# Optimization experiments

Hardware: AMD Instinct MI355X
Metric: run time of the kernel (lower is better)

Reference implementation:

```python
import jax, jax.numpy as jnp
import numpy as np

EPS = 1e-5

def _layernorm(x, g, b):
    m = jnp.mean(x, axis=-1, keepdims=True)
    v = jnp.mean((x - m) ** 2, axis=-1, keepdims=True)
    return (x - m) * jax.lax.rsqrt(v + EPS) * g + b

def setup_inputs() -> dict:
    N, D, R = 1024, 128, 64
    dist_mean = 60.0
    key = jax.random.key(0)
    ks = jax.random.split(key, 12)
    def lin(k, fan_in, shape):
        bound = 1.0 / np.sqrt(fan_in)
        return jax.random.uniform(k, shape, jnp.float32, -bound, bound)
    inp = {
        "node_emb": jax.random.normal(ks[0], (N, D), jnp.float32),
        # src_proj: Linear(D, R) + LayerNorm(R)
        "w_src": lin(ks[1], D, (R, D)), "b_src": lin(ks[2], D, (R,)),
        "g_src": jnp.ones((R,), jnp.float32), "be_src": jnp.zeros((R,), jnp.float32),
        # dst_proj: Linear(D, R) + LayerNorm(R)
        "w_dst": lin(ks[3], D, (R, D)), "b_dst": lin(ks[4], D, (R,)),
        "g_dst": jnp.ones((R,), jnp.float32), "be_dst": jnp.zeros((R,), jnp.float32),
        # scorer: Linear(3R, 2R) -> ReLU -> Linear(2R, R) -> ReLU -> Linear(R, 1)
        "w1": lin(ks[5], 3 * R, (2 * R, 3 * R)), "b1": lin(ks[6], 3 * R, (2 * R,)),
        "w2": lin(ks[7], 2 * R, (R, 2 * R)), "b2": lin(ks[8], 2 * R, (R,)),
        "w3": lin(ks[9], R, (1, R)) * 0.01, "b3": jnp.full((1,), dist_mean, jnp.float32),
    }
    return inp

def reference(node_emb, w_src, b_src, g_src, be_src, w_dst, b_dst, g_dst, be_dst,
              w1, b1, w2, b2, w3, b3):
    # src/dst projections: [N, R]
    src = jax.nn.relu(_layernorm(node_emb @ w_src.T + b_src, g_src, be_src))
    dst = jax.nn.relu(_layernorm(node_emb @ w_dst.T + b_dst, g_dst, be_dst))
    N = node_emb.shape[0]
    # broadcast pairwise features: [N, N, 3R]
    src_exp = jnp.broadcast_to(src[:, None, :], (N, N, src.shape[-1]))
    dst_exp = jnp.broadcast_to(dst[None, :, :], (N, N, dst.shape[-1]))
    pair = jnp.concatenate([src_exp, dst_exp, src_exp * dst_exp], axis=-1)
    h = jax.nn.relu(pair @ w1.T + b1)   # [N, N, 2R]
    h = jax.nn.relu(h @ w2.T + b2)      # [N, N, R]
    cost = (h @ w3.T + b3)[..., 0]      # [N, N]
    return cost
```

## Files before the change

kernel.cpp:

```cpp
#include <hip/hip_runtime.h>

typedef _Float16 half2v __attribute__((ext_vector_type(2)));
typedef _Float16 half8v __attribute__((ext_vector_type(8)));
typedef float f32x4 __attribute__((ext_vector_type(4)));
typedef unsigned uint2v __attribute__((ext_vector_type(2)));

__device__ inline half2v cvt_pk(float a, float b) {
    return __builtin_bit_cast(half2v, __builtin_amdgcn_cvt_pkrtz(a, b));
}
__device__ inline half2v pkmax0(half2v x) {
    half2v r;
    asm("v_pk_max_f16 %0, %1, 0" : "=v"(r) : "v"(x));
    return r;
}
__device__ inline unsigned short f16bits(float f) {
    _Float16 h = (_Float16)f;
    return __builtin_bit_cast(unsigned short, h);
}
__device__ inline unsigned packf16(float a, float b) {
    return (unsigned)f16bits(a) | ((unsigned)f16bits(b) << 16);
}
__device__ inline float lo16(unsigned u) {
    return (float)__builtin_bit_cast(_Float16, (unsigned short)(u & 0xffffu));
}
__device__ inline float hi16(unsigned u) {
    return (float)__builtin_bit_cast(_Float16, (unsigned short)(u >> 16));
}

__global__ __launch_bounds__(256) void proj_kernel(
    const float* __restrict__ node,
    const float* __restrict__ w_src, const float* __restrict__ b_src,
    const float* __restrict__ g_src, const float* __restrict__ be_src,
    const float* __restrict__ w_dst, const float* __restrict__ b_dst,
    const float* __restrict__ g_dst, const float* __restrict__ be_dst,
    const float* __restrict__ w1, const float* __restrict__ b1,
    const float* __restrict__ w2, const float* __restrict__ w3,
    unsigned short* __restrict__ src_f16, unsigned short* __restrict__ dst_f16,
    float* __restrict__ A1, unsigned short* __restrict__ B1h,
    unsigned short* __restrict__ w1c_frag, unsigned short* __restrict__ w2_frag,
    unsigned short* __restrict__ w3p)
{
    __shared__ unsigned sWh[64 * 65];
    __shared__ unsigned sw1h[128 * 33];
    __shared__ float snode[4][128];
    __shared__ float sy[4][64];

    const int tid = threadIdx.x;
    const int wloc = tid >> 6;
    const int lane = tid & 63;
    const int gw = blockIdx.x * 4 + wloc;
    const int row = gw & 1023;
    const int kind = gw >> 10;

    const float* W  = kind ? w_dst  : w_src;
    const float* Bv = kind ? b_dst  : b_src;
    const float* G  = kind ? g_dst  : g_src;
    const float* BE = kind ? be_dst : be_src;
    const int koff = kind * 64;

    #pragma unroll
    for (int u = 0; u < 16; u++) {
        int w = u * 256 + tid;
        int r = w >> 6, c2 = w & 63;
        float2 v = *(const float2*)(W + r * 128 + c2 * 2);
        sWh[r * 65 + c2] = packf16(v.x, v.y);
    }
    #pragma unroll
    for (int u = 0; u < 16; u++) {
        int w = u * 256 + tid;
        int r = w >> 5, c2 = w & 31;
        float2 v = *(const float2*)(w1 + (size_t)r * 192 + koff + c2 * 2);
        sw1h[r * 33 + c2] = packf16(v.x, v.y);
    }
    snode[wloc][lane]      = node[row * 128 + lane];
    snode[wloc][lane + 64] = node[row * 128 + 64 + lane];
    __syncthreads();

    float acc = Bv[lane];
    #pragma unroll 8
    for (int k2 = 0; k2 < 64; k2++) {
        unsigned wp = sWh[lane * 65 + k2];
        float2 nv = *(const float2*)&snode[wloc][2 * k2];
        acc += nv.x * lo16(wp) + nv.y * hi16(wp);
    }

    float s = acc;
    #pragma unroll
    for (int off = 32; off >= 1; off >>= 1) s += __shfl_xor(s, off);
    float mean = s * (1.0f / 64.0f);
    float d = acc - mean;
    float ss = d * d;
    #pragma unroll
    for (int off = 32; off >= 1; off >>= 1) ss += __shfl_xor(ss, off);
    float rstd = rsqrtf(ss * (1.0f / 64.0f) + 1e-5f);
    float y = fmaxf(d * rstd * G[lane] + BE[lane], 0.0f);

    unsigned short* obf = kind ? dst_f16 : src_f16;
    obf[row * 64 + lane] = f16bits(y);

    sy[wloc][lane] = y;
    __builtin_amdgcn_s_waitcnt(0);

    float a0 = kind ? 0.0f : b1[lane];
    float a1 = kind ? 0.0f : b1[lane + 64];
    #pragma unroll 8
    for (int k2 = 0; k2 < 32; k2++) {
        float2 yv = *(const float2*)&sy[wloc][2 * k2];
        unsigned wa = sw1h[lane * 33 + k2];
        unsigned wb = sw1h[(lane + 64) * 33 + k2];
        a0 += yv.x * lo16(wa) + yv.y * hi16(wa);
        a1 += yv.x * lo16(wb) + yv.y * hi16(wb);
    }
    if (kind == 0) {
        A1[row * 128 + lane] = a0;
        A1[row * 128 + lane + 64] = a1;
    } else {
        B1h[row * 128 + lane] = f16bits(a0);
        B1h[row * 128 + lane + 64] = f16bits(a1);
    }

    if (blockIdx.x < 8) {
        int t = blockIdx.x * 256 + threadIdx.x;
        int which = t >> 10;
        int idx = t & 1023;
        int f = idx >> 6, l = idx & 63;
        int lqq = l >> 4, lrr = l & 15;
        if (which == 0) {
            int mt = f >> 1, kt = f & 1;
            #pragma unroll
            for (int e = 0; e < 8; e++)
                w1c_frag[idx * 8 + e] =
                    f16bits(w1[(size_t)(mt * 16 + lrr) * 192 + 128 + kt * 32 + lqq * 8 + e]);
        } else {
            int mt2 = f >> 2, kt2 = f & 3;
            #pragma unroll
            for (int e = 0; e < 8; e++) {
                int col = (2 * kt2 + (e >> 2)) * 16 + lqq * 4 + (e & 3);
                w2_frag[idx * 8 + e] =
                    f16bits(w2[(size_t)(mt2 * 16 + lrr) * 128 + col]);
            }
        }
    } else if (blockIdx.x == 8 && threadIdx.x < 64) {
        int l = threadIdx.x;
        int kt = l >> 5, rem = l & 31, lqq = rem >> 3, ee = rem & 7;
        w3p[l] = f16bits(w3[(2 * kt + (ee >> 2)) * 16 + lqq * 4 + (ee & 3)]);
    }
}

__global__ __launch_bounds__(256, 2) void pair_kernel(
    const unsigned short* __restrict__ src_f16, const unsigned short* __restrict__ dst_f16,
    const float* __restrict__ A1, const unsigned short* __restrict__ B1h,
    const unsigned short* __restrict__ w1c_frag, const unsigned short* __restrict__ w2_frag,
    const unsigned short* __restrict__ w3p, const float* __restrict__ b2,
    const float* __restrict__ b3, float* __restrict__ out)
{
    __shared__ __align__(16) float sA1[32][128];
    __shared__ __align__(16) unsigned short sSrc[32][64];

    const int tid = threadIdx.x;
    const int wv = tid >> 6;
    const int lane = tid & 63;
    const int lq = lane >> 4, lr = lane & 15;
    const int i0 = blockIdx.y * 32, j0 = blockIdx.x * 32;
    const int ibase = (wv & 1) * 16;
    const int jbase = j0 + (wv >> 1) * 16;

    #pragma unroll
    for (int u = 0; u < 4; u++) {
        int idx = u * 256 + tid;
        int r = idx >> 5, c = (idx & 31) * 4;
        *(f32x4*)&sA1[r][c] = *(const f32x4*)(A1 + (size_t)(i0 + r) * 128 + c);
    }
    {
        int r = tid >> 3, c = (tid & 7) * 8;
        *(uint4*)&sSrc[r][c] = *(const uint4*)(src_f16 + (size_t)(i0 + r) * 64 + c);
    }

    half8v w1f[8][2], w2f[4][4], w3f[2];
    {
        const uint4* gw1 = (const uint4*)w1c_frag;
        #pragma unroll
        for (int mt = 0; mt < 8; mt++)
            #pragma unroll
            for (int kt = 0; kt < 2; kt++)
                w1f[mt][kt] = __builtin_bit_cast(half8v, gw1[(mt * 2 + kt) * 64 + lane]);
        const uint4* gw2 = (const uint4*)w2_frag;
        #pragma unroll
        for (int mt2 = 0; mt2 < 4; mt2++)
            #pragma unroll
            for (int kt = 0; kt < 4; kt++)
                w2f[mt2][kt] = __builtin_bit_cast(half8v, gw2[(mt2 * 4 + kt) * 64 + lane]);
        #pragma unroll
        for (int kt = 0; kt < 2; kt++)
            w3f[kt] = *(const half8v*)(w3p + kt * 32 + lq * 8);
    }
    f32x4 b2v[4];
    #pragma unroll
    for (int mt2 = 0; mt2 < 4; mt2++)
        b2v[mt2] = *(const f32x4*)(b2 + mt2 * 16 + lq * 4);
    const float b3s = b3[0];
    const f32x4 b3c = {b3s, b3s, b3s, b3s};

    const int j = jbase + lr;
    half8v dstf0, dstf1;
    {
        const uint4* drow = (const uint4*)(dst_f16 + (size_t)j * 64);
        dstf0 = __builtin_bit_cast(half8v, drow[lq]);
        dstf1 = __builtin_bit_cast(half8v, drow[4 + lq]);
    }
    half2v b1pk[8][2];
    #pragma unroll
    for (int mt = 0; mt < 8; mt++) {
        uint2v bl = *(const uint2v*)(B1h + (size_t)j * 128 + mt * 16 + lq * 4);
        b1pk[mt][0] = __builtin_bit_cast(half2v, bl[0]);
        b1pk[mt][1] = __builtin_bit_cast(half2v, bl[1]);
    }

    __syncthreads();

    for (int cc = 0; cc < 16; cc++) {
        const int i_loc = ibase + cc;
        const int i = i0 + i_loc;
        const half8v s0 = *(const half8v*)&sSrc[i_loc][lq * 8];
        const half8v s1 = *(const half8v*)&sSrc[i_loc][32 + lq * 8];
        f32x4 acc1[8];
        #pragma unroll
        for (int mt = 0; mt < 8; mt++)
            acc1[mt] = *(const f32x4*)&sA1[i_loc][mt * 16 + lq * 4];
        const half8v c0 = s0 * dstf0;
        const half8v c1 = s1 * dstf1;
        #pragma unroll
        for (int mt = 0; mt < 8; mt++) {
            acc1[mt] = __builtin_amdgcn_mfma_f32_16x16x32_f16(w1f[mt][0], c0, acc1[mt], 0, 0, 0);
            acc1[mt] = __builtin_amdgcn_mfma_f32_16x16x32_f16(w1f[mt][1], c1, acc1[mt], 0, 0, 0);
        }
        unsigned P[16];
        #pragma unroll
        for (int mt = 0; mt < 8; mt++) {
            half2v p0 = cvt_pk(acc1[mt][0], acc1[mt][1]) + b1pk[mt][0];
            half2v p1 = cvt_pk(acc1[mt][2], acc1[mt][3]) + b1pk[mt][1];
            P[mt * 2 + 0] = __builtin_bit_cast(unsigned, pkmax0(p0));
            P[mt * 2 + 1] = __builtin_bit_cast(unsigned, pkmax0(p1));
        }
        f32x4 acc2[4];
        {
            uint4 hb = {P[0], P[1], P[2], P[3]};
            half8v hf = __builtin_bit_cast(half8v, hb);
            #pragma unroll
            for (int mt2 = 0; mt2 < 4; mt2++)
                acc2[mt2] = __builtin_amdgcn_mfma_f32_16x16x32_f16(w2f[mt2][0], hf, b2v[mt2], 0, 0, 0);
        }
        #pragma unroll
        for (int kt = 1; kt < 4; kt++) {
            uint4 hb = {P[4 * kt], P[4 * kt + 1], P[4 * kt + 2], P[4 * kt + 3]};
            half8v hf = __builtin_bit_cast(half8v, hb);
            #pragma unroll
            for (int mt2 = 0; mt2 < 4; mt2++)
                acc2[mt2] = __builtin_amdgcn_mfma_f32_16x16x32_f16(w2f[mt2][kt], hf, acc2[mt2], 0, 0, 0);
        }
        unsigned P2[8];
        #pragma unroll
        for (int mt2 = 0; mt2 < 4; mt2++) {
            P2[mt2 * 2 + 0] = __builtin_bit_cast(unsigned, pkmax0(cvt_pk(acc2[mt2][0], acc2[mt2][1])));
            P2[mt2 * 2 + 1] = __builtin_bit_cast(unsigned, pkmax0(cvt_pk(acc2[mt2][2], acc2[mt2][3])));
        }
        uint4 h20 = {P2[0], P2[1], P2[2], P2[3]};
        uint4 h21 = {P2[4], P2[5], P2[6], P2[7]};
        f32x4 acc3 = __builtin_amdgcn_mfma_f32_16x16x32_f16(
            w3f[0], __builtin_bit_cast(half8v, h20), b3c, 0, 0, 0);
        acc3 = __builtin_amdgcn_mfma_f32_16x16x32_f16(
            w3f[1], __builtin_bit_cast(half8v, h21), acc3, 0, 0, 0);
        if (lane < 16)
            out[(size_t)i * 1024 + jbase + lane] = acc3[0];
    }
}

extern "C" void kernel_launch(void* const* d_in, const int* in_sizes, int n_in,
                              void* d_out, int out_size, void* d_ws, size_t ws_size,
                              hipStream_t stream) {
    (void)in_sizes; (void)n_in; (void)out_size; (void)ws_size;
    const float* node   = (const float*)d_in[0];
    const float* w_src  = (const float*)d_in[1];
    const float* b_src  = (const float*)d_in[2];
    const float* g_src  = (const float*)d_in[3];
    const float* be_src = (const float*)d_in[4];
    const float* w_dst  = (const float*)d_in[5];
    const float* b_dst  = (const float*)d_in[6];
    const float* g_dst  = (const float*)d_in[7];
    const float* be_dst = (const float*)d_in[8];
    const float* w1     = (const float*)d_in[9];
    const float* b1     = (const float*)d_in[10];
    const float* w2     = (const float*)d_in[11];
    const float* b2     = (const float*)d_in[12];
    const float* w3     = (const float*)d_in[13];
    const float* b3     = (const float*)d_in[14];

    char* ws = (char*)d_ws;
    unsigned short* src_f16  = (unsigned short*)(ws);
    unsigned short* dst_f16  = (unsigned short*)(ws + 131072);
    float*          A1       = (float*)(ws + 262144);
    unsigned short* B1h      = (unsigned short*)(ws + 786432);
    unsigned short* w1c_frag = (unsigned short*)(ws + 1310720);
    unsigned short* w2_frag  = (unsigned short*)(ws + 1327104);
    unsigned short* w3p      = (unsigned short*)(ws + 1343488);

    hipLaunchKernelGGL(proj_kernel, dim3(512), dim3(256), 0, stream,
                       node, w_src, b_src, g_src, be_src, w_dst, b_dst, g_dst, be_dst,
                       w1, b1, w2, w3, src_f16, dst_f16, A1, B1h,
                       w1c_frag, w2_frag, w3p);
    hipLaunchKernelGGL(pair_kernel, dim3(32, 32), dim3(256), 0, stream,
                       src_f16, dst_f16, A1, B1h, w1c_frag, w2_frag, w3p, b2, b3,
                       (float*)d_out);
}
```

Baseline: 42.41 us.

## Move B1/b2/w3 operands to LDS and replace final MFMA with shuffle reduction

Per-lane register copies of the B1 bias fragments and b2 are dropped; the pair kernel now stages B1 rows, b2 and w3 in shared memory and reads them inside the loop. The last linear layer (h @ w3) no longer uses an f16 MFMA. It becomes an fp32 dot product of the ReLU'd accumulators with w3, followed by two cross-lane shuffles. The aim is lower VGPR pressure and fewer MFMA and convert instructions, at the cost of extra LDS reads every iteration. The w3 repack step in the projection kernel is removed.

```diff
diff --git a/kernel.cpp b/kernel.cpp
--- a/kernel.cpp
+++ b/kernel.cpp
@@ -34,11 +34,10 @@
     const float* __restrict__ w_dst, const float* __restrict__ b_dst,
     const float* __restrict__ g_dst, const float* __restrict__ be_dst,
     const float* __restrict__ w1, const float* __restrict__ b1,
-    const float* __restrict__ w2, const float* __restrict__ w3,
+    const float* __restrict__ w2,
     unsigned short* __restrict__ src_f16, unsigned short* __restrict__ dst_f16,
     float* __restrict__ A1, unsigned short* __restrict__ B1h,
-    unsigned short* __restrict__ w1c_frag, unsigned short* __restrict__ w2_frag,
-    unsigned short* __restrict__ w3p)
+    unsigned short* __restrict__ w1c_frag, unsigned short* __restrict__ w2_frag)
 {
     __shared__ unsigned sWh[64 * 65];
     __shared__ unsigned sw1h[128 * 33];
@@ -140,10 +139,6 @@
                     f16bits(w2[(size_t)(mt2 * 16 + lrr) * 128 + col]);
             }
         }
-    } else if (blockIdx.x == 8 && threadIdx.x < 64) {
-        int l = threadIdx.x;
-        int kt = l >> 5, rem = l & 31, lqq = rem >> 3, ee = rem & 7;
-        w3p[l] = f16bits(w3[(2 * kt + (ee >> 2)) * 16 + lqq * 4 + (ee & 3)]);
     }
 }
 
@@ -151,11 +146,14 @@
     const unsigned short* __restrict__ src_f16, const unsigned short* __restrict__ dst_f16,
     const float* __restrict__ A1, const unsigned short* __restrict__ B1h,
     const unsigned short* __restrict__ w1c_frag, const unsigned short* __restrict__ w2_frag,
-    const unsigned short* __restrict__ w3p, const float* __restrict__ b2,
+    const float* __restrict__ b2, const float* __restrict__ w3,
     const float* __restrict__ b3, float* __restrict__ out)
 {
     __shared__ __align__(16) float sA1[32][128];
     __shared__ __align__(16) unsigned short sSrc[32][64];
+    __shared__ __align__(16) unsigned short sB1[32][136];
+    __shared__ __align__(16) float sB2[128];
+    __shared__ __align__(16) float sW3[64];
 
     const int tid = threadIdx.x;
     const int wv = tid >> 6;
@@ -163,7 +161,8 @@
     const int lq = lane >> 4, lr = lane & 15;
     const int i0 = blockIdx.y * 32, j0 = blockIdx.x * 32;
     const int ibase = (wv & 1) * 16;
-    const int jbase = j0 + (wv >> 1) * 16;
+    const int jl_base = (wv >> 1) * 16;
+    const int jbase = j0 + jl_base;
 
     #pragma unroll
     for (int u = 0; u < 4; u++) {
@@ -175,8 +174,16 @@
         int r = tid >> 3, c = (tid & 7) * 8;
         *(uint4*)&sSrc[r][c] = *(const uint4*)(src_f16 + (size_t)(i0 + r) * 64 + c);
     }
-
-    half8v w1f[8][2], w2f[4][4], w3f[2];
+    #pragma unroll
+    for (int u = 0; u < 2; u++) {
+        int idx = u * 256 + tid;
+        int r = idx >> 4, c = (idx & 15) * 8;
+        *(uint4*)&sB1[r][c] = *(const uint4*)(B1h + (size_t)(j0 + r) * 128 + c);
+    }
+    if (tid < 32) *(f32x4*)&sB2[tid * 4] = *(const f32x4*)(b2 + tid * 4);
+    else if (tid < 48) *(f32x4*)&sW3[(tid - 32) * 4] = *(const f32x4*)(w3 + (tid - 32) * 4);
+
+    half8v w1f[8][2], w2f[4][4];
     {
         const uint4* gw1 = (const uint4*)w1c_frag;
         #pragma unroll
@@ -190,16 +197,8 @@
             #pragma unroll
             for (int kt = 0; kt < 4; kt++)
                 w2f[mt2][kt] = __builtin_bit_cast(half8v, gw2[(mt2 * 4 + kt) * 64 + lane]);
-        #pragma unroll
-        for (int kt = 0; kt < 2; kt++)
-            w3f[kt] = *(const half8v*)(w3p + kt * 32 + lq * 8);
-    }
-    f32x4 b2v[4];
-    #pragma unroll
-    for (int mt2 = 0; mt2 < 4; mt2++)
-        b2v[mt2] = *(const f32x4*)(b2 + mt2 * 16 + lq * 4);
+    }
     const float b3s = b3[0];
-    const f32x4 b3c = {b3s, b3s, b3s, b3s};
 
     const int j = jbase + lr;
     half8v dstf0, dstf1;
@@ -208,13 +207,7 @@
         dstf0 = __builtin_bit_cast(half8v, drow[lq]);
         dstf1 = __builtin_bit_cast(half8v, drow[4 + lq]);
     }
-    half2v b1pk[8][2];
-    #pragma unroll
-    for (int mt = 0; mt < 8; mt++) {
-        uint2v bl = *(const uint2v*)(B1h + (size_t)j * 128 + mt * 16 + lq * 4);
-        b1pk[mt][0] = __builtin_bit_cast(half2v, bl[0]);
-        b1pk[mt][1] = __builtin_bit_cast(half2v, bl[1]);
-    }
+    const int jl = jl_base + lr;
 
     __syncthreads();
 
@@ -237,8 +230,9 @@
         unsigned P[16];
         #pragma unroll
         for (int mt = 0; mt < 8; mt++) {
-            half2v p0 = cvt_pk(acc1[mt][0], acc1[mt][1]) + b1pk[mt][0];
-            half2v p1 = cvt_pk(acc1[mt][2], acc1[mt][3]) + b1pk[mt][1];
+            uint2v bl = *(const uint2v*)&sB1[jl][mt * 16 + lq * 4];
+            half2v p0 = cvt_pk(acc1[mt][0], acc1[mt][1]) + __builtin_bit_cast(half2v, bl[0]);
+            half2v p1 = cvt_pk(acc1[mt][2], acc1[mt][3]) + __builtin_bit_cast(half2v, bl[1]);
             P[mt * 2 + 0] = __builtin_bit_cast(unsigned, pkmax0(p0));
             P[mt * 2 + 1] = __builtin_bit_cast(unsigned, pkmax0(p1));
         }
@@ -247,8 +241,10 @@
             uint4 hb = {P[0], P[1], P[2], P[3]};
             half8v hf = __builtin_bit_cast(half8v, hb);
             #pragma unroll
-            for (int mt2 = 0; mt2 < 4; mt2++)
-                acc2[mt2] = __builtin_amdgcn_mfma_f32_16x16x32_f16(w2f[mt2][0], hf, b2v[mt2], 0, 0, 0);
+            for (int mt2 = 0; mt2 < 4; mt2++) {
+                f32x4 b2t = *(const f32x4*)&sB2[mt2 * 16 + lq * 4];
+                acc2[mt2] = __builtin_amdgcn_mfma_f32_16x16x32_f16(w2f[mt2][0], hf, b2t, 0, 0, 0);
+            }
         }
         #pragma unroll
         for (int kt = 1; kt < 4; kt++) {
@@ -258,20 +254,18 @@
             for (int mt2 = 0; mt2 < 4; mt2++)
                 acc2[mt2] = __builtin_amdgcn_mfma_f32_16x16x32_f16(w2f[mt2][kt], hf, acc2[mt2], 0, 0, 0);
         }
-        unsigned P2[8];
+        float part = 0.0f;
         #pragma unroll
         for (int mt2 = 0; mt2 < 4; mt2++) {
-            P2[mt2 * 2 + 0] = __builtin_bit_cast(unsigned, pkmax0(cvt_pk(acc2[mt2][0], acc2[mt2][1])));
-            P2[mt2 * 2 + 1] = __builtin_bit_cast(unsigned, pkmax0(cvt_pk(acc2[mt2][2], acc2[mt2][3])));
-        }
-        uint4 h20 = {P2[0], P2[1], P2[2], P2[3]};
-        uint4 h21 = {P2[4], P2[5], P2[6], P2[7]};
-        f32x4 acc3 = __builtin_amdgcn_mfma_f32_16x16x32_f16(
-            w3f[0], __builtin_bit_cast(half8v, h20), b3c, 0, 0, 0);
-        acc3 = __builtin_amdgcn_mfma_f32_16x16x32_f16(
-            w3f[1], __builtin_bit_cast(half8v, h21), acc3, 0, 0, 0);
+            f32x4 w3t = *(const f32x4*)&sW3[mt2 * 16 + lq * 4];
+            #pragma unroll
+            for (int r = 0; r < 4; r++)
+                part += fmaxf(acc2[mt2][r], 0.0f) * w3t[r];
+        }
+        part += __shfl_xor(part, 16);
+        part += __shfl_xor(part, 32);
         if (lane < 16)
-            out[(size_t)i * 1024 + jbase + lane] = acc3[0];
+            out[(size_t)i * 1024 + jbase + lane] = part + b3s;
     }
 }
 
@@ -302,13 +296,12 @@
     unsigned short* B1h      = (unsigned short*)(ws + 786432);
     unsigned short* w1c_frag = (unsigned short*)(ws + 1310720);
     unsigned short* w2_frag  = (unsigned short*)(ws + 1327104);
-    unsigned short* w3p      = (unsigned short*)(ws + 1343488);
 
     hipLaunchKernelGGL(proj_kernel, dim3(512), dim3(256), 0, stream,
                        node, w_src, b_src, g_src, be_src, w_dst, b_dst, g_dst, be_dst,
-                       w1, b1, w2, w3, src_f16, dst_f16, A1, B1h,
-                       w1c_frag, w2_frag, w3p);
+                       w1, b1, w2, src_f16, dst_f16, A1, B1h,
+                       w1c_frag, w2_frag);
     hipLaunchKernelGGL(pair_kernel, dim3(32, 32), dim3(256), 0, stream,
-                       src_f16, dst_f16, A1, B1h, w1c_frag, w2_frag, w3p, b2, b3,
+                       src_f16, dst_f16, A1, B1h, w1c_frag, w2_frag, b2, w3, b3,
                        (float*)d_out);
 }
```

After: 46.22 us. 9.0% more time.

## Stream weight fragments from global and batch four rows per MFMA group

Applied to the files above, without the earlier changes.

Weight fragments for the three MLP layers are no longer kept in registers for the whole kernel. They are reloaded from global memory (L1/L2-cached) inside the loop. The row loop now handles four i-rows at a time, so each loaded weight fragment feeds four independent MFMA chains, giving more instruction-level parallelism and hiding MFMA latency. The risk is extra global/cache load traffic per group, and the new larger accumulator arrays (acc1[4][8], acc2[4][4]) may offset the register savings.

```diff
diff --git a/kernel.cpp b/kernel.cpp
--- a/kernel.cpp
+++ b/kernel.cpp
@@ -176,31 +176,6 @@
         *(uint4*)&sSrc[r][c] = *(const uint4*)(src_f16 + (size_t)(i0 + r) * 64 + c);
     }
 
-    half8v w1f[8][2], w2f[4][4], w3f[2];
-    {
-        const uint4* gw1 = (const uint4*)w1c_frag;
-        #pragma unroll
-        for (int mt = 0; mt < 8; mt++)
-            #pragma unroll
-            for (int kt = 0; kt < 2; kt++)
-                w1f[mt][kt] = __builtin_bit_cast(half8v, gw1[(mt * 2 + kt) * 64 + lane]);
-        const uint4* gw2 = (const uint4*)w2_frag;
-        #pragma unroll
-        for (int mt2 = 0; mt2 < 4; mt2++)
-            #pragma unroll
-            for (int kt = 0; kt < 4; kt++)
-                w2f[mt2][kt] = __builtin_bit_cast(half8v, gw2[(mt2 * 4 + kt) * 64 + lane]);
-        #pragma unroll
-        for (int kt = 0; kt < 2; kt++)
-            w3f[kt] = *(const half8v*)(w3p + kt * 32 + lq * 8);
-    }
-    f32x4 b2v[4];
-    #pragma unroll
-    for (int mt2 = 0; mt2 < 4; mt2++)
-        b2v[mt2] = *(const f32x4*)(b2 + mt2 * 16 + lq * 4);
-    const float b3s = b3[0];
-    const f32x4 b3c = {b3s, b3s, b3s, b3s};
-
     const int j = jbase + lr;
     half8v dstf0, dstf1;
     {
@@ -215,63 +190,104 @@
         b1pk[mt][0] = __builtin_bit_cast(half2v, bl[0]);
         b1pk[mt][1] = __builtin_bit_cast(half2v, bl[1]);
     }
+    f32x4 b2v[4];
+    #pragma unroll
+    for (int mt2 = 0; mt2 < 4; mt2++)
+        b2v[mt2] = *(const f32x4*)(b2 + mt2 * 16 + lq * 4);
+    const float b3s = b3[0];
+    const f32x4 b3c = {b3s, b3s, b3s, b3s};
+
+    const uint4* gw1 = (const uint4*)w1c_frag;
+    const uint4* gw2 = (const uint4*)w2_frag;
 
     __syncthreads();
 
-    for (int cc = 0; cc < 16; cc++) {
-        const int i_loc = ibase + cc;
-        const int i = i0 + i_loc;
-        const half8v s0 = *(const half8v*)&sSrc[i_loc][lq * 8];
-        const half8v s1 = *(const half8v*)&sSrc[i_loc][32 + lq * 8];
-        f32x4 acc1[8];
-        #pragma unroll
-        for (int mt = 0; mt < 8; mt++)
-            acc1[mt] = *(const f32x4*)&sA1[i_loc][mt * 16 + lq * 4];
-        const half8v c0 = s0 * dstf0;
-        const half8v c1 = s1 * dstf1;
+    for (int g = 0; g < 4; g++) {
+        const int ib = ibase + g * 4;
+
+        half8v c0[4], c1[4];
+        f32x4 acc1[4][8];
+        #pragma unroll
+        for (int ii = 0; ii < 4; ii++) {
+            const int i_loc = ib + ii;
+            half8v s0 = *(const half8v*)&sSrc[i_loc][lq * 8];
+            half8v s1 = *(const half8v*)&sSrc[i_loc][32 + lq * 8];
+            c0[ii] = s0 * dstf0;
+            c1[ii] = s1 * dstf1;
+            #pragma unroll
+            for (int mt = 0; mt < 8; mt++)
+                acc1[ii][mt] = *(const f32x4*)&sA1[i_loc][mt * 16 + lq * 4];
+        }
+
         #pragma unroll
         for (int mt = 0; mt < 8; mt++) {
-            acc1[mt] = __builtin_amdgcn_mfma_f32_16x16x32_f16(w1f[mt][0], c0, acc1[mt], 0, 0, 0);
-            acc1[mt] = __builtin_amdgcn_mfma_f32_16x16x32_f16(w1f[mt][1], c1, acc1[mt], 0, 0, 0);
-        }
-        unsigned P[16];
-        #pragma unroll
-        for (int mt = 0; mt < 8; mt++) {
-            half2v p0 = cvt_pk(acc1[mt][0], acc1[mt][1]) + b1pk[mt][0];
-            half2v p1 = cvt_pk(acc1[mt][2], acc1[mt][3]) + b1pk[mt][1];
-            P[mt * 2 + 0] = __builtin_bit_cast(unsigned, pkmax0(p0));
-            P[mt * 2 + 1] = __builtin_bit_cast(unsigned, pkmax0(p1));
-        }
-        f32x4 acc2[4];
-        {
-            uint4 hb = {P[0], P[1], P[2], P[3]};
-            half8v hf = __builtin_bit_cast(half8v, hb);
-            #pragma unroll
-            for (int mt2 = 0; mt2 < 4; mt2++)
-                acc2[mt2] = __builtin_amdgcn_mfma_f32_16x16x32_f16(w2f[mt2][0], hf, b2v[mt2], 0, 0, 0);
-        }
-        #pragma unroll
-        for (int kt = 1; kt < 4; kt++) {
-            uint4 hb = {P[4 * kt], P[4 * kt + 1], P[4 * kt + 2], P[4 * kt + 3]};
-            half8v hf = __builtin_bit_cast(half8v, hb);
-            #pragma unroll
-            for (int mt2 = 0; mt2 < 4; mt2++)
-                acc2[mt2] = __builtin_amdgcn_mfma_f32_16x16x32_f16(w2f[mt2][kt], hf, acc2[mt2], 0, 0, 0);
-        }
-        unsigned P2[8];
-        #pragma unroll
-        for (int mt2 = 0; mt2 < 4; mt2++) {
-            P2[mt2 * 2 + 0] = __builtin_bit_cast(unsigned, pkmax0(cvt_pk(acc2[mt2][0], acc2[mt2][1])));
-            P2[mt2 * 2 + 1] = __builtin_bit_cast(unsigned, pkmax0(cvt_pk(acc2[mt2][2], acc2[mt2][3])));
-        }
-        uint4 h20 = {P2[0], P2[1], P2[2], P2[3]};
-        uint4 h21 = {P2[4], P2[5], P2[6], P2[7]};
-        f32x4 acc3 = __builtin_amdgcn_mfma_f32_16x16x32_f16(
-            w3f[0], __builtin_bit_cast(half8v, h20), b3c, 0, 0, 0);
-        acc3 = __builtin_amdgcn_mfma_f32_16x16x32_f16(
-            w3f[1], __builtin_bit_cast(half8v, h21), acc3, 0, 0, 0);
-        if (lane < 16)
-            out[(size_t)i * 1024 + jbase + lane] = acc3[0];
+            half8v wa = __builtin_bit_cast(half8v, gw1[(mt * 2 + 0) * 64 + lane]);
+            #pragma unroll
+            for (int ii = 0; ii < 4; ii++)
+                acc1[ii][mt] = __builtin_amdgcn_mfma_f32_16x16x32_f16(wa, c0[ii], acc1[ii][mt], 0, 0, 0);
+            half8v wb = __builtin_bit_cast(half8v, gw1[(mt * 2 + 1) * 64 + lane]);
+            #pragma unroll
+            for (int ii = 0; ii < 4; ii++)
+                acc1[ii][mt] = __builtin_amdgcn_mfma_f32_16x16x32_f16(wb, c1[ii], acc1[ii][mt], 0, 0, 0);
+        }
+
+        unsigned P[4][16];
+        #pragma unroll
+        for (int ii = 0; ii < 4; ii++)
+            #pragma unroll
+            for (int mt = 0; mt < 8; mt++) {
+                half2v p0 = cvt_pk(acc1[ii][mt][0], acc1[ii][mt][1]) + b1pk[mt][0];
+                half2v p1 = cvt_pk(acc1[ii][mt][2], acc1[ii][mt][3]) + b1pk[mt][1];
+                P[ii][mt * 2 + 0] = __builtin_bit_cast(unsigned, pkmax0(p0));
+                P[ii][mt * 2 + 1] = __builtin_bit_cast(unsigned, pkmax0(p1));
+            }
+
+        f32x4 acc2[4][4];
+        #pragma unroll
+        for (int kt = 0; kt < 4; kt++) {
+            half8v hf[4];
+            #pragma unroll
+            for (int ii = 0; ii < 4; ii++) {
+                uint4 hb = {P[ii][4 * kt], P[ii][4 * kt + 1], P[ii][4 * kt + 2], P[ii][4 * kt + 3]};
+                hf[ii] = __builtin_bit_cast(half8v, hb);
+            }
+            #pragma unroll
+            for (int mt2 = 0; mt2 < 4; mt2++) {
+                half8v w2l = __builtin_bit_cast(half8v, gw2[(mt2 * 4 + kt) * 64 + lane]);
+                #pragma unroll
+                for (int ii = 0; ii < 4; ii++) {
+                    f32x4 cin = (kt == 0) ? b2v[mt2] : acc2[ii][mt2];
+                    acc2[ii][mt2] = __builtin_amdgcn_mfma_f32_16x16x32_f16(w2l, hf[ii], cin, 0, 0, 0);
+                }
+            }
+        }
+
+        #pragma unroll
+        for (int half = 0; half < 2; half++) {
+            half8v w3l = *(const half8v*)(w3p + half * 32 + lq * 8);
+            #pragma unroll
+            for (int ii = 0; ii < 4; ii++) {
+                unsigned q0 = __builtin_bit_cast(unsigned,
+                    pkmax0(cvt_pk(acc2[ii][half * 2 + 0][0], acc2[ii][half * 2 + 0][1])));
+                unsigned q1 = __builtin_bit_cast(unsigned,
+                    pkmax0(cvt_pk(acc2[ii][half * 2 + 0][2], acc2[ii][half * 2 + 0][3])));
+                unsigned q2 = __builtin_bit_cast(unsigned,
+                    pkmax0(cvt_pk(acc2[ii][half * 2 + 1][0], acc2[ii][half * 2 + 1][1])));
+                unsigned q3 = __builtin_bit_cast(unsigned,
+                    pkmax0(cvt_pk(acc2[ii][half * 2 + 1][2], acc2[ii][half * 2 + 1][3])));
+                uint4 hb = {q0, q1, q2, q3};
+                half8v hq = __builtin_bit_cast(half8v, hb);
+                if (half == 0)
+                    acc1[ii][0] = __builtin_amdgcn_mfma_f32_16x16x32_f16(w3l, hq, b3c, 0, 0, 0);
+                else
+                    acc1[ii][0] = __builtin_amdgcn_mfma_f32_16x16x32_f16(w3l, hq, acc1[ii][0], 0, 0, 0);
+            }
+        }
+        #pragma unroll
+        for (int ii = 0; ii < 4; ii++) {
+            if (lane < 16)
+                out[(size_t)(i0 + ib + ii) * 1024 + jbase + lane] = acc1[ii][0][0];
+        }
     }
 }
 
```

Measured after the change: 55.08 us. 29.9% more time.
